# Kernel optimization log

Measured on AMD Instinct MI355X. Metric: run time of the kernel, lower is better.

Reference implementation:

```python
import jax, jax.numpy as jnp
import numpy as np

LN_EPS = 1e-5


def setup_inputs() -> dict:
    key = jax.random.key(0)
    k1, k2, k3, k4 = jax.random.split(key, 4)
    B, S, H, NH = 32, 256, 4096, 16
    scale = (2.0 ** 0.5) * ((3.0 / H) ** 0.5)
    inp = jax.random.normal(k1, (B, S, H), dtype=jnp.float32)
    mask = jax.random.randint(k2, (B, S), 0, 2, dtype=jnp.int32)  # 1 = padded key
    weight = jnp.ones((H,), dtype=jnp.float32)
    bias = jnp.zeros((H,), dtype=jnp.float32)
    qkv = jax.random.normal(k3, (H, 3 * H), dtype=jnp.float32) * scale
    o = jax.random.normal(k4, (H, H), dtype=jnp.float32) * scale
    return {"inp": inp, "mask": mask, "weight": weight, "bias": bias,
            "qkv": qkv, "o": o, "isPre": 1}


def _layer_norm(x, weight, bias):
    mu = jnp.mean(x, axis=-1, keepdims=True)
    var = jnp.mean(jnp.square(x - mu), axis=-1, keepdims=True)
    return (x - mu) * jax.lax.rsqrt(var + LN_EPS) * weight + bias


def _mha(x, mask, weight, bias, qkv, o, isPre, head_num=16):
    B, S, H = x.shape
    D = H // head_num
    xn = _layer_norm(x, weight, bias) if isPre else x
    # fused QKV projection: [B,S,3H]
    proj = jnp.einsum('bsh,hk->bsk', xn, qkv)
    q, k, v = jnp.split(proj, 3, axis=-1)
    q = q.reshape(B, S, head_num, D)
    k = k.reshape(B, S, head_num, D)
    v = v.reshape(B, S, head_num, D)
    scores = jnp.einsum('bqnd,bknd->bnqk', q, k) / jnp.sqrt(jnp.float32(D))
    # mask[b,k]==1 -> key k is padding, exclude from softmax
    neg = jnp.finfo(scores.dtype).min
    scores = jnp.where(mask[:, None, None, :] != 0, neg, scores)
    attn = jax.nn.softmax(scores, axis=-1)
    ctx = jnp.einsum('bnqk,bknd->bqnd', attn, v).reshape(B, S, H)
    out = jnp.einsum('bsh,ho->bso', ctx, o)
    if not isPre:
        out = _layer_norm(out, weight, bias)
    return out


def reference(inp, mask, weight, bias, qkv, o, isPre):
    return _mha(inp, mask, weight, bias, qkv, o, bool(isPre))
```

## Files before the change

kernel.cpp:

```cpp
#include <hip/hip_runtime.h>
#include <stdint.h>

typedef unsigned short u16;
typedef short bf16x8 __attribute__((ext_vector_type(8)));
typedef float f32x4 __attribute__((ext_vector_type(4)));

#define MFMA16(a, b, c) __builtin_amdgcn_mfma_f32_16x16x32_bf16((a), (b), (c), 0, 0, 0)

#define GLOAD_LDS16(gp, lp)                                                        \
  __builtin_amdgcn_global_load_lds((const __attribute__((address_space(1))) void*)(gp), \
                                   (__attribute__((address_space(3))) void*)(lp), 16, 0, 0)

#define BARRIER asm volatile("s_barrier" ::: "memory")
#define WAITV(n) asm volatile("s_waitcnt vmcnt(" #n ")" ::: "memory")
#define WAITL0 asm volatile("s_waitcnt lgkmcnt(0)" ::: "memory")

__device__ __forceinline__ u16 f2bf(float x) {
  union { float f; uint32_t u; } v; v.f = x;
  uint32_t r = (v.u + 0x7FFFu + ((v.u >> 16) & 1u)) >> 16;
  return (u16)r;
}

__global__ __launch_bounds__(256) void transpose_bf16(const float* __restrict__ in,
                                                      u16* __restrict__ out, int R, int C) {
  __shared__ float tile[32][33];
  int nCt = C >> 5;
  int bid = blockIdx.x;
  int r0 = (bid / nCt) << 5, c0 = (bid % nCt) << 5;
  int t = threadIdx.x;
  int r = t >> 3, cc = (t & 7) << 2;
  float4 v = *reinterpret_cast<const float4*>(in + (size_t)(r0 + r) * C + c0 + cc);
  tile[r][cc] = v.x; tile[r][cc + 1] = v.y; tile[r][cc + 2] = v.z; tile[r][cc + 3] = v.w;
  __syncthreads();
  int c = t >> 3, rr = (t & 7) << 2;
  ushort4 u;
  u.x = f2bf(tile[rr][c]);     u.y = f2bf(tile[rr + 1][c]);
  u.z = f2bf(tile[rr + 2][c]); u.w = f2bf(tile[rr + 3][c]);
  *reinterpret_cast<ushort4*>(out + (size_t)(c0 + c) * R + r0 + rr) = u;
}

__global__ __launch_bounds__(256) void ln_bf16(const float* __restrict__ in,
                                               const float* __restrict__ w,
                                               const float* __restrict__ bia,
                                               u16* __restrict__ out) {
  int row = blockIdx.x, t = threadIdx.x;
  const float* x = in + (size_t)row * 4096;
  float4 v[4];
  float s = 0.f, sq = 0.f;
#pragma unroll
  for (int i = 0; i < 4; i++) {
    v[i] = *reinterpret_cast<const float4*>(x + i * 1024 + t * 4);
    s  += v[i].x + v[i].y + v[i].z + v[i].w;
    sq += v[i].x * v[i].x + v[i].y * v[i].y + v[i].z * v[i].z + v[i].w * v[i].w;
  }
#pragma unroll
  for (int off = 32; off > 0; off >>= 1) { s += __shfl_down(s, off); sq += __shfl_down(sq, off); }
  __shared__ float red[8];
  int wid = t >> 6, lane = t & 63;
  if (lane == 0) { red[wid] = s; red[4 + wid] = sq; }
  __syncthreads();
  if (t == 0) {
    float st = red[0] + red[1] + red[2] + red[3];
    float sqt = red[4] + red[5] + red[6] + red[7];
    float mu = st * (1.f / 4096.f);
    float var = sqt * (1.f / 4096.f) - mu * mu;
    red[0] = mu; red[1] = rsqrtf(var + 1e-5f);
  }
  __syncthreads();
  float mu = red[0], rs = red[1];
#pragma unroll
  for (int i = 0; i < 4; i++) {
    float4 wv = *reinterpret_cast<const float4*>(w + i * 1024 + t * 4);
    float4 bv = *reinterpret_cast<const float4*>(bia + i * 1024 + t * 4);
    ushort4 u;
    u.x = f2bf((v[i].x - mu) * rs * wv.x + bv.x);
    u.y = f2bf((v[i].y - mu) * rs * wv.y + bv.y);
    u.z = f2bf((v[i].z - mu) * rs * wv.z + bv.z);
    u.w = f2bf((v[i].w - mu) * rs * wv.w + bv.w);
    *reinterpret_cast<ushort4*>(out + (size_t)row * 4096 + i * 1024 + t * 4) = u;
  }
}


#define LDA8(AR, Ab, mh) do {                                                     \
  _Pragma("unroll")                                                               \
  for (int mf = 0; mf < 4; mf++) {                                                \
    int lr = (mh)*128 + wm64 + mf*16 + llo;                                       \
    const char* rb = (Ab) + lr*128;                                               \
    int sw = (lr & 7) << 4;                                                       \
    AR[mf*2+0] = *reinterpret_cast<const bf16x8*>(rb + ((lhi16) ^ sw));           \
    AR[mf*2+1] = *reinterpret_cast<const bf16x8*>(rb + ((64 + lhi16) ^ sw));      \
  }                                                                               \
} while (0)

#define LDB4(BR, Bb, nh) do {                                                     \
  _Pragma("unroll")                                                               \
  for (int nf = 0; nf < 2; nf++) {                                                \
    int lr = (nh)*128 + wn32 + nf*16 + llo;                                       \
    const char* rb = (Bb) + lr*128;                                               \
    int sw = (lr & 7) << 4;                                                       \
    BR[nf*2+0] = *reinterpret_cast<const bf16x8*>(rb + ((lhi16) ^ sw));           \
    BR[nf*2+1] = *reinterpret_cast<const bf16x8*>(rb + ((64 + lhi16) ^ sw));      \
  }                                                                               \
} while (0)

#define MMAQ(AR, BR, mh, nh) do {                                                 \
  _Pragma("unroll")                                                               \
  for (int mf = 0; mf < 4; mf++)                                                  \
    _Pragma("unroll")                                                             \
    for (int nf = 0; nf < 2; nf++) {                                              \
      acc[(mh)*4+mf][(nh)*2+nf] = MFMA16(AR[mf*2+0], BR[nf*2+0], acc[(mh)*4+mf][(nh)*2+nf]); \
      acc[(mh)*4+mf][(nh)*2+nf] = MFMA16(AR[mf*2+1], BR[nf*2+1], acc[(mh)*4+mf][(nh)*2+nf]); \
    }                                                                             \
} while (0)

#define STAGE(isB, h, cbuf, ktile) do {                                           \
  const u16* g_ = (isB) ? Bt : A;                                                 \
  int base0_ = (isB) ? n0 : m0;                                                   \
  char* lb_ = smc + (cbuf)*65536 + (isB)*32768 + (h)*16384;                       \
  _Pragma("unroll")                                                               \
  for (int i_ = 0; i_ < 2; i_++) {                                                \
    int L_ = i_*512 + t;                                                          \
    int lr_ = (h)*128 + (L_ >> 3);                                                \
    int sl_ = (L_ & 7) ^ (lr_ & 7);                                               \
    int r_ = (isB) ? (((lr_ & 128) >> 2) | ((lr_ & 96) << 1) | (lr_ & 31))        \
                   : ((lr_ & 63) | ((lr_ & 64) << 1) | ((lr_ & 128) >> 1));       \
    GLOAD_LDS16(g_ + (size_t)(base0_ + r_) * K + (ktile)*64 + sl_*8, lb_ + L_*16);\
  }                                                                               \
} while (0)

#define TILE2(tt, S1, S2, W2) do {                                                \
  int c_ = (tt) & 1;                                                              \
  const char* Ab = smc + c_ * 65536;                                              \
  const char* Bb = Ab + 32768;                                                    \
          \
  LDA8(aR, Ab, 0); LDB4(b0R, Bb, 0); LDB4(b1R, Bb, 1);                            \
  if (S1) { STAGE(1, 0, c_ ^ 1, (tt) + 1); STAGE(0, 1, c_ ^ 1, (tt) + 1); }       \
  __builtin_amdgcn_s_setprio(1);                                                  \
  MMAQ(aR, b0R, 0, 0); MMAQ(aR, b1R, 0, 1);                                       \
  __builtin_amdgcn_s_setprio(0);                                                  \
  WAITL0; BARRIER;                                                                \
                                     \
  LDA8(aR, Ab, 1);                                                                \
  if (S2) { STAGE(0, 0, c_, (tt) + 2); STAGE(1, 1, c_, (tt) + 2); }               \
  __builtin_amdgcn_s_setprio(1);                                                  \
  MMAQ(aR, b1R, 1, 1); MMAQ(aR, b0R, 1, 0);                                       \
  __builtin_amdgcn_s_setprio(0);                                                  \
  WAITV(W2); WAITL0; BARRIER;                                                     \
} while (0)

template <int EPI>
__global__ __launch_bounds__(512, 2) void gemm256(const u16* __restrict__ A, const u16* __restrict__ Bt,
                                                  void* __restrict__ Cout, u16* __restrict__ vT,
                                                  int M, int N, int K, int nbn) {
  __shared__ u16 sm[65536];
  char* smc = (char*)sm;
  int bid = blockIdx.x;
  int s = bid >> 8, local = bid & 255;
  int xcd = local & 7, j = local >> 3;
  int trow = ((xcd >> 1) << 2) + (j >> 3);
  int tcol = ((xcd & 1) << 3) + (j & 7);
  int nsc = nbn >> 4;
  int sr = s / nsc, sc = s - sr * nsc;
  int tm = (sr << 4) + trow, tn = (sc << 4) + tcol;
  int m0 = tm << 8, n0 = tn << 8;
  int t = threadIdx.x;
  int w = t >> 6, lane = t & 63;
  int wm = w >> 2, wn = w & 3;
  int llo = lane & 15, lhi = lane >> 4;
  int wm64 = wm << 6, wn32 = wn << 5, lhi16 = lhi << 4;
  f32x4 acc[8][4] = {};
  bf16x8 aR[8], b0R[4], b1R[4];
  int NT = K >> 6;
  STAGE(0, 0, 0, 0); STAGE(1, 0, 0, 0); STAGE(1, 1, 0, 0); STAGE(0, 1, 0, 0);
  STAGE(0, 0, 1, 1); STAGE(1, 1, 1, 1);
  WAITV(4); BARRIER;
#pragma unroll 1
  for (int tt = 0; tt < NT - 2; ++tt) TILE2(tt, 1, 1, 4);
  TILE2(NT - 2, 1, 0, 0);
  TILE2(NT - 1, 0, 0, 0);
  if (EPI == 2) {
    float* C = (float*)Cout;
#pragma unroll
    for (int mi = 0; mi < 8; mi++)
#pragma unroll
      for (int ni = 0; ni < 4; ni++) {
        int m = m0 + wm * 128 + mi * 16 + lhi * 4;
        int n = n0 + wn * 64 + ni * 16 + llo;
#pragma unroll
        for (int r = 0; r < 4; r++) C[(size_t)(m + r) * N + n] = acc[mi][ni][r];
      }
  } else {
    if (n0 < 8192) {
      u16* qkb = (u16*)Cout;
#pragma unroll
      for (int mi = 0; mi < 8; mi++)
#pragma unroll
        for (int ni = 0; ni < 4; ni++) {
          int m = m0 + wm * 128 + mi * 16 + lhi * 4;
          int n = n0 + wn * 64 + ni * 16 + llo;
#pragma unroll
          for (int r = 0; r < 4; r++) qkb[(size_t)(m + r) * 8192 + n] = f2bf(acc[mi][ni][r]);
        }
    } else {
#pragma unroll
      for (int mi = 0; mi < 8; mi++)
#pragma unroll
        for (int ni = 0; ni < 4; ni++) {
          int m = m0 + wm * 128 + mi * 16 + lhi * 4;
          int n_ = n0 + wn * 64 + ni * 16 + llo - 8192;
          int h = n_ >> 8, d = n_ & 255;
          int b = m >> 8, s2 = m & 255;
          ushort4 u;
          u.x = f2bf(acc[mi][ni][0]); u.y = f2bf(acc[mi][ni][1]);
          u.z = f2bf(acc[mi][ni][2]); u.w = f2bf(acc[mi][ni][3]);
          *reinterpret_cast<ushort4*>(vT + ((size_t)((b << 4) + h) * 256 + d) * 256 + s2) = u;
        }
    }
  }
}

__global__ __launch_bounds__(256) void attn_kernel(const u16* __restrict__ qk,
                                                   const u16* __restrict__ vT,
                                                   const int* __restrict__ mask,
                                                   u16* __restrict__ ctx) {
  __shared__ u16 KV[64 * 256];
  __shared__ u16 P[64 * 256];
  __shared__ float maskf[256];
  int bx = blockIdx.x;
  int qt = bx & 3, h = (bx >> 2) & 15, b = bx >> 6;
  int t = threadIdx.x, wid = t >> 6, lane = t & 63, llo = lane & 15, lhi = lane >> 4;
  maskf[t] = mask[(b << 8) + t] ? -1e30f : 0.0f;
  bf16x8 qf[8];
  {
    const u16* qrow = qk + (size_t)((b << 8) + (qt << 6) + (wid << 4) + llo) * 8192 + (h << 8);
#pragma unroll
    for (int c = 0; c < 8; c++)
      qf[c] = *reinterpret_cast<const bf16x8*>(qrow + (lhi << 3) + (c << 5));
  }
  f32x4 sacc[16] = {};
#pragma unroll 1
  for (int kt = 0; kt < 4; kt++) {
    __syncthreads();
#pragma unroll
    for (int i = 0; i < 8; i++) {
      int G = (i << 8) + t;
      int key = G >> 5, g = G & 31;
      int gs = g ^ (key & 7);
      const u16* src = qk + (size_t)((b << 8) + (kt << 6) + key) * 8192 + 4096 + (h << 8) + (gs << 3);
      GLOAD_LDS16(src, (char*)KV + (G << 4));
    }
    __syncthreads();
#pragma unroll
    for (int nf = 0; nf < 4; nf++) {
      int kl = (nf << 4) + llo;
      const char* kb = (const char*)KV + (kl << 9);
      int sw = (kl & 7) << 4;
#pragma unroll
      for (int c = 0; c < 8; c++) {
        bf16x8 kf = *reinterpret_cast<const bf16x8*>(kb + (((lhi << 4) + (c << 6)) ^ sw));
        sacc[kt * 4 + nf] = MFMA16(qf[c], kf, sacc[kt * 4 + nf]);
      }
    }
  }
  float madd[16];
#pragma unroll
  for (int f = 0; f < 16; f++)
    madd[f] = maskf[((f >> 2) << 6) + ((f & 3) << 4) + llo];
  float mx[4] = {-3e38f, -3e38f, -3e38f, -3e38f};
#pragma unroll
  for (int f = 0; f < 16; f++)
#pragma unroll
    for (int r = 0; r < 4; r++) {
      float sv = sacc[f][r] * 0.0625f + madd[f];
      sacc[f][r] = sv;
      mx[r] = fmaxf(mx[r], sv);
    }
#pragma unroll
  for (int r = 0; r < 4; r++)
#pragma unroll
    for (int d = 1; d < 16; d <<= 1) mx[r] = fmaxf(mx[r], __shfl_xor(mx[r], d));
  float sum[4] = {0.f, 0.f, 0.f, 0.f};
#pragma unroll
  for (int f = 0; f < 16; f++)
#pragma unroll
    for (int r = 0; r < 4; r++) {
      float p = __expf(sacc[f][r] - mx[r]);
      sacc[f][r] = p;
      sum[r] += p;
    }
#pragma unroll
  for (int r = 0; r < 4; r++)
#pragma unroll
    for (int d = 1; d < 16; d <<= 1) sum[r] += __shfl_xor(sum[r], d);
  float rin[4];
#pragma unroll
  for (int r = 0; r < 4; r++) rin[r] = 1.f / sum[r];
#pragma unroll
  for (int r = 0; r < 4; r++) {
    int q = (wid << 4) + (lhi << 2) + r;
    char* pb = (char*)P + (q << 9);
    int sw = (q & 7) << 4;
#pragma unroll
    for (int f = 0; f < 16; f++) {
      int key = ((f >> 2) << 6) + ((f & 3) << 4) + llo;
      *reinterpret_cast<u16*>(pb + ((key << 1) ^ sw)) = f2bf(sacc[f][r] * rin[r]);
    }
  }
  f32x4 cacc[16] = {};
#pragma unroll 1
  for (int kt = 0; kt < 4; kt++) {
    __syncthreads();
#pragma unroll
    for (int i = 0; i < 8; i++) {
      int G = (i << 8) + t;
      int d = G >> 3, g = G & 7;
      int gs = g ^ (d & 7);
      const u16* src = vT + ((size_t)((b << 4) + h) * 256 + d) * 256 + (kt << 6) + (gs << 3);
      GLOAD_LDS16(src, (char*)KV + (G << 4));
    }
    __syncthreads();
    bf16x8 pf[2];
    {
      int q = (wid << 4) + llo;
      const char* pb = (const char*)P + (q << 9);
      int sw = (q & 7) << 4;
#pragma unroll
      for (int c = 0; c < 2; c++)
        pf[c] = *reinterpret_cast<const bf16x8*>(pb + (((kt << 7) + (c << 6) + (lhi << 4)) ^ sw));
    }
#pragma unroll
    for (int mf = 0; mf < 16; mf++) {
      int dl = (mf << 4) + llo;
      const char* vb = (const char*)KV + (dl << 7);
      int sw = (dl & 7) << 4;
#pragma unroll
      for (int c = 0; c < 2; c++) {
        bf16x8 vf = *reinterpret_cast<const bf16x8*>(vb + (((lhi << 4) + (c << 6)) ^ sw));
        cacc[mf] = MFMA16(vf, pf[c], cacc[mf]);
      }
    }
  }
  int token = (b << 8) + (qt << 6) + (wid << 4) + llo;
  u16* crow = ctx + (size_t)token * 4096 + (h << 8);
#pragma unroll
  for (int mf = 0; mf < 16; mf++) {
    ushort4 u;
    u.x = f2bf(cacc[mf][0]); u.y = f2bf(cacc[mf][1]);
    u.z = f2bf(cacc[mf][2]); u.w = f2bf(cacc[mf][3]);
    *reinterpret_cast<ushort4*>(crow + (mf << 4) + (lhi << 2)) = u;
  }
}

extern "C" void kernel_launch(void* const* d_in, const int* in_sizes, int n_in,
                              void* d_out, int out_size, void* d_ws, size_t ws_size,
                              hipStream_t stream) {
  const float* inp  = (const float*)d_in[0];
  const int*   mask = (const int*)d_in[1];
  const float* w    = (const float*)d_in[2];
  const float* bia  = (const float*)d_in[3];
  const float* qkvw = (const float*)d_in[4];
  const float* ow   = (const float*)d_in[5];
  const size_t MB = 1024ull * 1024ull;
  if (ws_size < 352 * MB) return;
  char* ws = (char*)d_ws;
  u16* xn   = (u16*)(ws);
  u16* qkvT = (u16*)(ws + 64 * MB);
  u16* qk   = (u16*)(ws + 160 * MB);
  u16* vT   = (u16*)(ws + 288 * MB);
  u16* oT   = (u16*)(ws + 64 * MB);
  u16* ctx  = (u16*)(ws);
  float* out = (float*)d_out;

  transpose_bf16<<<49152, 256, 0, stream>>>(qkvw, qkvT, 4096, 12288);
  ln_bf16<<<8192, 256, 0, stream>>>(inp, w, bia, xn);
  gemm256<1><<<1536, 512, 0, stream>>>(xn, qkvT, (void*)qk, vT, 8192, 12288, 4096, 48);
  transpose_bf16<<<16384, 256, 0, stream>>>(ow, oT, 4096, 4096);
  attn_kernel<<<2048, 256, 0, stream>>>(qk, vT, mask, ctx);
  gemm256<2><<<512, 512, 0, stream>>>(ctx, oT, (void*)out, nullptr, 8192, 4096, 4096, 16);
}
```

Measured before the change: 1.265 ms.

## Restructure GEMM main loop with register double-buffering and sched barriers; widen transpose tiles

The GEMM main loop now double-buffers the A fragments in registers (a0R/a1R). It prefetches the next tile's first fragments during the current MFMAs and stages the whole next K-tile at the start of each iteration instead of splitting staging across halves. Explicit sched_group_barrier patterns interleave MFMA, global-to-LDS loads and LDS reads, and the prefetch depth drops from two tiles to one with a full vmcnt(0) wait. The weight transpose kernel moves to 64x64 tiles with 16-byte stores to cut block count and improve write width. The risks are more register pressure and less global-load latency hiding from the shallower prefetch.

```diff
diff --git a/kernel.cpp b/kernel.cpp
--- a/kernel.cpp
+++ b/kernel.cpp
@@ -4,6 +4,7 @@
 typedef unsigned short u16;
 typedef short bf16x8 __attribute__((ext_vector_type(8)));
 typedef float f32x4 __attribute__((ext_vector_type(4)));
+typedef unsigned short u16x8 __attribute__((ext_vector_type(8)));
 
 #define MFMA16(a, b, c) __builtin_amdgcn_mfma_f32_16x16x32_bf16((a), (b), (c), 0, 0, 0)
 
@@ -14,6 +15,7 @@
 #define BARRIER asm volatile("s_barrier" ::: "memory")
 #define WAITV(n) asm volatile("s_waitcnt vmcnt(" #n ")" ::: "memory")
 #define WAITL0 asm volatile("s_waitcnt lgkmcnt(0)" ::: "memory")
+#define SGB(mask, n) __builtin_amdgcn_sched_group_barrier((mask), (n), 0)
 
 __device__ __forceinline__ u16 f2bf(float x) {
   union { float f; uint32_t u; } v; v.f = x;
@@ -23,20 +25,29 @@
 
 __global__ __launch_bounds__(256) void transpose_bf16(const float* __restrict__ in,
                                                       u16* __restrict__ out, int R, int C) {
-  __shared__ float tile[32][33];
-  int nCt = C >> 5;
+  __shared__ float tile[64][65];
+  int nCt = C >> 6;
   int bid = blockIdx.x;
-  int r0 = (bid / nCt) << 5, c0 = (bid % nCt) << 5;
+  int r0 = (bid / nCt) << 6, c0 = (bid % nCt) << 6;
   int t = threadIdx.x;
-  int r = t >> 3, cc = (t & 7) << 2;
-  float4 v = *reinterpret_cast<const float4*>(in + (size_t)(r0 + r) * C + c0 + cc);
-  tile[r][cc] = v.x; tile[r][cc + 1] = v.y; tile[r][cc + 2] = v.z; tile[r][cc + 3] = v.w;
+  int r = t >> 2, cg = (t & 3) << 4;
+  const float* src = in + (size_t)(r0 + r) * C + c0 + cg;
+#pragma unroll
+  for (int i = 0; i < 4; i++) {
+    float4 v = *reinterpret_cast<const float4*>(src + (i << 2));
+    tile[r][cg + (i << 2) + 0] = v.x; tile[r][cg + (i << 2) + 1] = v.y;
+    tile[r][cg + (i << 2) + 2] = v.z; tile[r][cg + (i << 2) + 3] = v.w;
+  }
   __syncthreads();
-  int c = t >> 3, rr = (t & 7) << 2;
-  ushort4 u;
-  u.x = f2bf(tile[rr][c]);     u.y = f2bf(tile[rr + 1][c]);
-  u.z = f2bf(tile[rr + 2][c]); u.w = f2bf(tile[rr + 3][c]);
-  *reinterpret_cast<ushort4*>(out + (size_t)(c0 + c) * R + r0 + rr) = u;
+  int c = t >> 2, rg = (t & 3) << 4;
+  u16* dst = out + (size_t)(c0 + c) * R + r0 + rg;
+#pragma unroll
+  for (int i = 0; i < 2; i++) {
+    u16x8 o8;
+#pragma unroll
+    for (int j2 = 0; j2 < 8; j2++) o8[j2] = f2bf(tile[rg + (i << 3) + j2][c]);
+    *reinterpret_cast<u16x8*>(dst + (i << 3)) = o8;
+  }
 }
 
 __global__ __launch_bounds__(256) void ln_bf16(const float* __restrict__ in,
@@ -129,24 +140,45 @@
   }                                                                               \
 } while (0)
 
-#define TILE2(tt, S1, S2, W2) do {                                                \
+#define TILEBODY(tt, SN) do {                                                     \
   int c_ = (tt) & 1;                                                              \
   const char* Ab = smc + c_ * 65536;                                              \
   const char* Bb = Ab + 32768;                                                    \
-          \
-  LDA8(aR, Ab, 0); LDB4(b0R, Bb, 0); LDB4(b1R, Bb, 1);                            \
-  if (S1) { STAGE(1, 0, c_ ^ 1, (tt) + 1); STAGE(0, 1, c_ ^ 1, (tt) + 1); }       \
+  const char* Abn = smc + (c_ ^ 1) * 65536;                                       \
+  const char* Bbn = Abn + 32768;                                                  \
+                       \
+  if (SN) { STAGE(0, 0, c_ ^ 1, (tt) + 1); STAGE(0, 1, c_ ^ 1, (tt) + 1);         \
+            STAGE(1, 0, c_ ^ 1, (tt) + 1); STAGE(1, 1, c_ ^ 1, (tt) + 1); }       \
+  LDB4(b1R, Bb, 1);                                                               \
+  LDA8(a1R, Ab, 1);                                                               \
   __builtin_amdgcn_s_setprio(1);                                                  \
-  MMAQ(aR, b0R, 0, 0); MMAQ(aR, b1R, 0, 1);                                       \
+  MMAQ(a0R, b0R, 0, 0);                                                           \
+  MMAQ(a1R, b0R, 1, 0);                                                           \
   __builtin_amdgcn_s_setprio(0);                                                  \
+  if (SN) {                                                                       \
+    _Pragma("unroll")                                                             \
+    for (int i_ = 0; i_ < 4; i_++) { SGB(0x100, 3); SGB(0x20, 2); SGB(0x8, 8); }  \
+  } else {                                                                        \
+    _Pragma("unroll")                                                             \
+    for (int i_ = 0; i_ < 4; i_++) { SGB(0x100, 3); SGB(0x8, 8); }                \
+  }                                                                               \
+  WAITV(0); BARRIER;                                                              \
+     \
+  if (SN) { LDB4(b0R, Bbn, 0); }                                                  \
+  __builtin_amdgcn_s_setprio(1);                                                  \
+  MMAQ(a0R, b1R, 0, 1);                                                           \
+  __builtin_amdgcn_s_setprio(0);                                                  \
+  if (SN) { LDA8(a0R, Abn, 0); }                                                  \
+  __builtin_amdgcn_s_setprio(1);                                                  \
+  MMAQ(a1R, b1R, 1, 1);                                                           \
+  __builtin_amdgcn_s_setprio(0);                                                  \
+  if (SN) {                                                                       \
+    _Pragma("unroll")                                                             \
+    for (int i_ = 0; i_ < 4; i_++) { SGB(0x100, 1); SGB(0x8, 4); }                \
+    _Pragma("unroll")                                                             \
+    for (int i_ = 0; i_ < 4; i_++) { SGB(0x100, 2); SGB(0x8, 4); }                \
+  }                                                                               \
   WAITL0; BARRIER;                                                                \
-                                     \
-  LDA8(aR, Ab, 1);                                                                \
-  if (S2) { STAGE(0, 0, c_, (tt) + 2); STAGE(1, 1, c_, (tt) + 2); }               \
-  __builtin_amdgcn_s_setprio(1);                                                  \
-  MMAQ(aR, b1R, 1, 1); MMAQ(aR, b0R, 1, 0);                                       \
-  __builtin_amdgcn_s_setprio(0);                                                  \
-  WAITV(W2); WAITL0; BARRIER;                                                     \
 } while (0)
 
 template <int EPI>
@@ -170,15 +202,15 @@
   int llo = lane & 15, lhi = lane >> 4;
   int wm64 = wm << 6, wn32 = wn << 5, lhi16 = lhi << 4;
   f32x4 acc[8][4] = {};
-  bf16x8 aR[8], b0R[4], b1R[4];
+  bf16x8 a0R[8], a1R[8], b0R[4], b1R[4];
   int NT = K >> 6;
-  STAGE(0, 0, 0, 0); STAGE(1, 0, 0, 0); STAGE(1, 1, 0, 0); STAGE(0, 1, 0, 0);
-  STAGE(0, 0, 1, 1); STAGE(1, 1, 1, 1);
-  WAITV(4); BARRIER;
+  STAGE(0, 0, 0, 0); STAGE(0, 1, 0, 0); STAGE(1, 0, 0, 0); STAGE(1, 1, 0, 0);
+  WAITV(0); BARRIER;
+  LDB4(b0R, smc + 32768, 0);
+  LDA8(a0R, smc, 0);
 #pragma unroll 1
-  for (int tt = 0; tt < NT - 2; ++tt) TILE2(tt, 1, 1, 4);
-  TILE2(NT - 2, 1, 0, 0);
-  TILE2(NT - 1, 0, 0, 0);
+  for (int tt = 0; tt < NT - 1; ++tt) TILEBODY(tt, 1);
+  TILEBODY(NT - 1, 0);
   if (EPI == 2) {
     float* C = (float*)Cout;
 #pragma unroll
@@ -372,10 +404,10 @@
   u16* ctx  = (u16*)(ws);
   float* out = (float*)d_out;
 
-  transpose_bf16<<<49152, 256, 0, stream>>>(qkvw, qkvT, 4096, 12288);
+  transpose_bf16<<<12288, 256, 0, stream>>>(qkvw, qkvT, 4096, 12288);
   ln_bf16<<<8192, 256, 0, stream>>>(inp, w, bia, xn);
   gemm256<1><<<1536, 512, 0, stream>>>(xn, qkvT, (void*)qk, vT, 8192, 12288, 4096, 48);
-  transpose_bf16<<<16384, 256, 0, stream>>>(ow, oT, 4096, 4096);
+  transpose_bf16<<<4096, 256, 0, stream>>>(ow, oT, 4096, 4096);
   attn_kernel<<<2048, 256, 0, stream>>>(qk, vT, mask, ctx);
   gemm256<2><<<512, 512, 0, stream>>>(ctx, oT, (void*)out, nullptr, 8192, 4096, 4096, 16);
 }
```

New measurement: 1.396 ms. +10.3%, slower.
